# Kernel tuning notes

Measured on AMD Instinct MI355X. Metric: run time of the kernel, lower is better.

Reference implementation:

```python
import jax, jax.numpy as jnp
import numpy as np

N_HEAD = 12
ROPE_BASE = 10000.0


def rotate_half(x):
    h = x.shape[-1] // 2
    x1, x2 = x[..., :h], x[..., h:]
    return jnp.concatenate((-x2, x1), axis=-1)


def rope_cos_sin(T, head_dim, dtype):
    inv_freq = 1.0 / (ROPE_BASE ** (jnp.arange(0, head_dim, 2, dtype=jnp.float32) / head_dim))
    t = jnp.arange(T, dtype=jnp.float32)
    freqs = jnp.einsum('i,j->ij', t, inv_freq)          # [T, head_dim/2]
    emb = jnp.concatenate((freqs, freqs), axis=-1)       # [T, head_dim]
    return jnp.cos(emb).astype(dtype), jnp.sin(emb).astype(dtype)


def setup_inputs() -> dict:
    key = jax.random.key(0)
    ks = jax.random.split(key, 5)
    B, T, C = 1, 4096, 768
    return {
        'x': jax.random.normal(ks[0], (B, T, C), dtype=jnp.float32),
        'w_attn': jax.random.normal(ks[1], (C, 3 * C), dtype=jnp.float32) * (1.0 / np.sqrt(C)),
        'b_attn': jax.random.normal(ks[2], (3 * C,), dtype=jnp.float32) * 0.02,
        'w_proj': jax.random.normal(ks[3], (C, C), dtype=jnp.float32) * (1.0 / np.sqrt(C)),
        'b_proj': jax.random.normal(ks[4], (C,), dtype=jnp.float32) * 0.02,
    }


def reference(x, w_attn, b_attn, w_proj, b_proj):
    B, T, C = x.shape
    H = N_HEAD
    hd = C // H

    qkv = x @ w_attn + b_attn                            # [B, T, 3C]
    q, k, v = jnp.split(qkv, 3, axis=-1)
    q = q.reshape(B, T, H, hd)
    k = k.reshape(B, T, H, hd)
    v = v.reshape(B, T, H, hd)

    cos, sin = rope_cos_sin(T, hd, x.dtype)              # [T, hd]
    cos = cos[None, :, None, :]
    sin = sin[None, :, None, :]
    q = q * cos + rotate_half(q) * sin
    k = k * cos + rotate_half(k) * sin

    # [B, H, T, hd]
    q = q.transpose(0, 2, 1, 3)
    k = k.transpose(0, 2, 1, 3)
    v = v.transpose(0, 2, 1, 3)

    att = jnp.einsum('bhtd,bhsd->bhts', q, k) * (1.0 / np.sqrt(hd))
    causal_mask = jnp.triu(jnp.ones((T, T), dtype=bool), k=1)
    att = jnp.where(causal_mask, -jnp.inf, att)
    att = jax.nn.softmax(att, axis=-1)

    y = jnp.einsum('bhts,bhsd->bhtd', att, v)            # [B, H, T, hd]
    y = y.transpose(0, 2, 1, 3).reshape(B, T, C)
    return y @ w_proj + b_proj
```

## Files before the change

### kernel.cpp

```cpp
#include <hip/hip_runtime.h>
#include <hip/hip_bf16.h>
#include <math.h>

using bf16 = __hip_bfloat16;
typedef __bf16 bf16x8_t __attribute__((ext_vector_type(8)));
typedef float f32x4_t __attribute__((ext_vector_type(4)));

static __device__ __forceinline__ f32x4_t mfma16(bf16x8_t a, bf16x8_t b, f32x4_t c) {
    return __builtin_amdgcn_mfma_f32_16x16x32_bf16(a, b, c, 0, 0, 0);
}

#if __has_builtin(__builtin_amdgcn_exp2f)
#define EXP2F __builtin_amdgcn_exp2f
#else
#define EXP2F exp2f
#endif

static __device__ __forceinline__ void sincos_rev(float rev, float* s, float* c) {
    float f = rev - floorf(rev);
#if __has_builtin(__builtin_amdgcn_sinf) && __has_builtin(__builtin_amdgcn_cosf)
    *s = __builtin_amdgcn_sinf(f);
    *c = __builtin_amdgcn_cosf(f);
#else
    float th = f * 6.2831853071795864f;
    *s = __sinf(th); *c = __cosf(th);
#endif
}

static __device__ __forceinline__ void async16(bf16* lds, const bf16* g) {
    __builtin_amdgcn_global_load_lds(
        (const __attribute__((address_space(1))) unsigned int*)g,
        (__attribute__((address_space(3))) unsigned int*)lds, 16, 0, 0);
}

static __device__ __forceinline__ int detect_bf16(const unsigned short* u16) {
    const int lane = threadIdx.x & 63;
    int sane = 0;
#pragma unroll
    for (int j = 0; j < 4; ++j) {
        const unsigned short u = u16[2 * (lane * 4 + j)];
        const int e = (u >> 7) & 0xFF;
        if (u == 0 || (e >= 100 && e <= 150)) sane++;
    }
#pragma unroll
    for (int off = 1; off <= 32; off <<= 1) sane += __shfl_xor(sane, off);
    return (sane * 2 >= 256) ? 1 : 0;
}

static __device__ __forceinline__ float bias_at(const void* b, int i, int isbf) {
    return isbf ? __bfloat162float(((const bf16*)b)[i]) : ((const float*)b)[i];
}

static __device__ __forceinline__ void transpose_tile(
    const void* in, bf16* out, int in_ld, int out_ld, int bx, int by,
    int isbf, bf16 (*tile)[72]) {
    const int c0 = bx * 64, r0 = by * 64;
    const int tid = threadIdx.x;
    for (int c = tid; c < 512; c += 256) {
        const int r = c >> 3, co = (c & 7) << 3;
        if (isbf) {
            *reinterpret_cast<float4*>(&tile[r][co]) =
                *reinterpret_cast<const float4*>((const bf16*)in + (size_t)(r0 + r) * in_ld + c0 + co);
        } else {
            const float* f = (const float*)in + (size_t)(r0 + r) * in_ld + c0 + co;
            const float4 a = *reinterpret_cast<const float4*>(f);
            const float4 b = *reinterpret_cast<const float4*>(f + 4);
            tile[r][co + 0] = __float2bfloat16(a.x); tile[r][co + 1] = __float2bfloat16(a.y);
            tile[r][co + 2] = __float2bfloat16(a.z); tile[r][co + 3] = __float2bfloat16(a.w);
            tile[r][co + 4] = __float2bfloat16(b.x); tile[r][co + 5] = __float2bfloat16(b.y);
            tile[r][co + 6] = __float2bfloat16(b.z); tile[r][co + 7] = __float2bfloat16(b.w);
        }
    }
    __syncthreads();
    for (int c = tid; c < 512; c += 256) {
        const int r = c >> 3, co = (c & 7) << 3;
        union { float4 v; bf16 e[8]; } u;
#pragma unroll
        for (int j = 0; j < 8; ++j) u.e[j] = tile[co + j][r];
        *reinterpret_cast<float4*>(out + (size_t)(c0 + r) * out_ld + r0 + co) = u.v;
    }
}

__global__ __launch_bounds__(256) void prep_kernel(
    const void* __restrict__ x, const void* __restrict__ w_attn,
    const void* __restrict__ w_proj, bf16* __restrict__ xb,
    bf16* __restrict__ wAT, bf16* __restrict__ wPT) {
    __shared__ bf16 tile[64][72];
    const int isbf = detect_bf16((const unsigned short*)x);
    const int b = blockIdx.x;
    if (b < 432) {
        transpose_tile(w_attn, wAT, 2304, 768, b % 36, b / 36, isbf, tile);
    } else if (b < 576) {
        const int bb = b - 432;
        transpose_tile(w_proj, wPT, 768, 768, bb % 12, bb / 12, isbf, tile);
    } else {
        const int i = ((b - 576) * 256 + threadIdx.x) * 8;
        if (isbf) {
            *reinterpret_cast<float4*>(xb + i) =
                *reinterpret_cast<const float4*>((const bf16*)x + i);
        } else {
            const float* f = (const float*)x + i;
            const float4 a = *reinterpret_cast<const float4*>(f);
            const float4 c = *reinterpret_cast<const float4*>(f + 4);
            union { float4 v; bf16 e[8]; } u;
            u.e[0] = __float2bfloat16(a.x); u.e[1] = __float2bfloat16(a.y);
            u.e[2] = __float2bfloat16(a.z); u.e[3] = __float2bfloat16(a.w);
            u.e[4] = __float2bfloat16(c.x); u.e[5] = __float2bfloat16(c.y);
            u.e[6] = __float2bfloat16(c.z); u.e[7] = __float2bfloat16(c.w);
            *reinterpret_cast<float4*>(xb + i) = u.v;
        }
    }
}

template <int MI>
__global__ __launch_bounds__(256, MI == 4 ? 3 : 4) void gemm_kernel(
    const bf16* __restrict__ A, const bf16* __restrict__ Bt,
    const void* __restrict__ bias, bf16* __restrict__ C,
    bf16* __restrict__ VtOut, const unsigned short* __restrict__ xdet,
    int N, int K, int mode, int flexout) {
    constexpr int MT = MI * 32;
    __shared__ bf16 smem[(MT + 128) * 64];
    bf16* sa = smem;
    bf16* sb = smem + MT * 64;
    const int tid = threadIdx.x, lane = tid & 63, w = tid >> 6;
    const int wm = w >> 1, wn = w & 1, quad = lane >> 4, l16 = lane & 15;
    const int m0 = blockIdx.y * MT, n0 = blockIdx.x * 128;
    const int strow = lane >> 3, stslot = lane & 7;

    const bf16* ag[MI]; const bf16* bgp[4];
#pragma unroll
    for (int i = 0; i < MI; ++i) {
        const int r = (w * MI + i) * 8 + strow;
        ag[i] = A + (size_t)(m0 + r) * K + (stslot ^ (r & 7)) * 8;
    }
#pragma unroll
    for (int i = 0; i < 4; ++i) {
        const int r = (w * 4 + i) * 8 + strow;
        bgp[i] = Bt + (size_t)(n0 + r) * K + (stslot ^ (r & 7)) * 8;
    }

    f32x4_t acc[MI][4];
#pragma unroll
    for (int i = 0; i < MI; ++i)
#pragma unroll
        for (int j = 0; j < 4; ++j) acc[i][j] = (f32x4_t){0.f, 0.f, 0.f, 0.f};

    for (int k0 = 0; k0 < K; k0 += 64) {
        __syncthreads();
#pragma unroll
        for (int i = 0; i < MI; ++i) async16(&sa[(w * MI + i) * 512], ag[i] + k0);
#pragma unroll
        for (int i = 0; i < 4; ++i)  async16(&sb[(w * 4 + i) * 512], bgp[i] + k0);
        __asm__ __volatile__("s_waitcnt vmcnt(0)" ::: "memory");
        __syncthreads();

#pragma unroll
        for (int kk = 0; kk < 2; ++kk) {
            bf16x8_t af[MI], bf_[4];
#pragma unroll
            for (int mi = 0; mi < MI; ++mi) {
                const int r = wm * (MI * 16) + mi * 16 + l16;
                af[mi] = *reinterpret_cast<const bf16x8_t*>(
                    &sa[r * 64 + (((kk * 4 + quad) ^ (r & 7)) << 3)]);
            }
#pragma unroll
            for (int ni = 0; ni < 4; ++ni) {
                const int r = wn * 64 + ni * 16 + l16;
                bf_[ni] = *reinterpret_cast<const bf16x8_t*>(
                    &sb[r * 64 + (((kk * 4 + quad) ^ (r & 7)) << 3)]);
            }
#pragma unroll
            for (int mi = 0; mi < MI; ++mi)
#pragma unroll
                for (int ni = 0; ni < 4; ++ni)
                    acc[mi][ni] = mfma16(af[mi], bf_[ni], acc[mi][ni]);
        }
    }

    const int isbf = detect_bf16(xdet);
    const int f32out = flexout && !isbf;
    const int colbase = n0 + wn * 64;
    const int rowbase = m0 + wm * (MI * 16);
    if (mode == 1 && colbase < 1536) {
        const bool isq = colbase < 768;
        const float QS = 0.18033688011112042f;
#pragma unroll
        for (int ni = 0; ni < 2; ++ni) {
            const int d = ni * 16 + l16;
            const int col_lo = colbase + d, col_hi = col_lo + 32;
            const float blo = bias_at(bias, col_lo, isbf);
            const float bhi = bias_at(bias, col_hi, isbf);
            const float invf_rev = powf(10000.0f, -(float)d * (1.0f / 32.0f)) * 0.15915494309189535f;
#pragma unroll
            for (int mi = 0; mi < MI; ++mi) {
#pragma unroll
                for (int rg = 0; rg < 4; ++rg) {
                    const int t = rowbase + mi * 16 + quad * 4 + rg;
                    float sv, cv;
                    sincos_rev((float)t * invf_rev, &sv, &cv);
                    const float lo = acc[mi][ni][rg] + blo;
                    const float hi = acc[mi][ni + 2][rg] + bhi;
                    float nlo = lo * cv - hi * sv;
                    float nhi = hi * cv + lo * sv;
                    if (isq) { nlo *= QS; nhi *= QS; }
                    C[(size_t)t * N + col_lo] = __float2bfloat16(nlo);
                    C[(size_t)t * N + col_hi] = __float2bfloat16(nhi);
                }
            }
        }
    } else if (mode == 1) {
        if constexpr (MI == 4) {
            __syncthreads();
            bf16* T = smem + w * 2304;
            const int vcb = colbase - 1536;
#pragma unroll
            for (int pass = 0; pass < 2; ++pass) {
                if (pass) __asm__ __volatile__("s_waitcnt lgkmcnt(0)" ::: "memory");
#pragma unroll
                for (int nl = 0; nl < 2; ++nl) {
                    const int ni = pass * 2 + nl;
                    const float b = bias_at(bias, colbase + ni * 16 + l16, isbf);
                    const int dh = nl * 16 + l16;
#pragma unroll
                    for (int rg = 0; rg < 4; ++rg) {
                        union { int2 v; bf16 e[4]; } pk;
#pragma unroll
                        for (int mi = 0; mi < 4; ++mi)
                            pk.e[mi] = __float2bfloat16(acc[mi][ni][rg] + b);
                        *reinterpret_cast<int2*>(&T[dh * 72 + quad * 16 + rg * 4]) = pk.v;
                    }
                }
                __asm__ __volatile__("s_waitcnt lgkmcnt(0)" ::: "memory");
#pragma unroll
                for (int s = 0; s < 4; ++s) {
                    const int dh = s * 8 + (lane >> 3);
                    const int pj = lane & 7;
                    const float4 vv = *reinterpret_cast<const float4*>(&T[dh * 72 + pj * 8]);
                    *reinterpret_cast<float4*>(
                        &VtOut[(size_t)(vcb + pass * 32 + dh) * 4096 + rowbase + pj * 8]) = vv;
                }
            }
        }
    } else {
#pragma unroll
        for (int ni = 0; ni < 4; ++ni) {
            const int col = colbase + ni * 16 + l16;
            const float b = bias_at(bias, col, isbf);
#pragma unroll
            for (int mi = 0; mi < MI; ++mi) {
#pragma unroll
                for (int rg = 0; rg < 4; ++rg) {
                    const int t = rowbase + mi * 16 + quad * 4 + rg;
                    const float v = acc[mi][ni][rg] + b;
                    if (f32out) ((float*)C)[(size_t)t * N + col] = v;
                    else        C[(size_t)t * N + col] = __float2bfloat16(v);
                }
            }
        }
    }
}

__global__ __launch_bounds__(128, 3) void attn_kernel(
    const bf16* __restrict__ qkv, const bf16* __restrict__ Vt,
    bf16* __restrict__ ybuf, bf16* __restrict__ po, float* __restrict__ pl) {
    const int h = blockIdx.y;
    const int bx = blockIdx.x;
    int qt, c, nc;
    if (bx < 16)      { qt = bx;                 c = 0;             nc = 1; }
    else if (bx < 48) { qt = 16 + (bx - 16) / 2; c = (bx - 16) % 2; nc = 2; }
    else if (bx < 96) { qt = 32 + (bx - 48) / 3; c = (bx - 48) % 3; nc = 3; }
    else              { qt = 48 + (bx - 96) / 4; c = (bx - 96) % 4; nc = 4; }
    const int kt0 = c * 16;
    const int kt1 = min(kt0 + 16, qt + 1);

    const int tid = threadIdx.x, lane = tid & 63, w = tid >> 6;
    const int quad = lane >> 4, l16 = lane & 15, sw = l16 & 7;

    __shared__ bf16 Kt[4096];
    __shared__ bf16 Vs[4096];
    __shared__ bf16 Pt[2][2][16][72];

    const int strow = lane >> 3, stslot = lane & 7;
    const bf16* kg[4]; const bf16* vg[4];
#pragma unroll
    for (int i = 0; i < 4; ++i) {
        const int ch = w * 4 + i;
        const int key = ch * 8 + strow;
        kg[i] = qkv + (size_t)key * 2304 + 768 + h * 64 + (stslot ^ (key & 7)) * 8;
        const int d = ch * 8 + strow;
        vg[i] = Vt + (size_t)(h * 64 + d) * 4096 + (stslot ^ (d & 7)) * 8;
    }

    const int qbase = qt * 64 + w * 32;
    bf16x8_t qf[2][2];
#pragma unroll
    for (int f = 0; f < 2; ++f)
#pragma unroll
        for (int kc = 0; kc < 2; ++kc)
            qf[f][kc] = *reinterpret_cast<const bf16x8_t*>(
                qkv + (size_t)(qbase + f * 16 + l16) * 2304 + h * 64 + kc * 32 + quad * 8);

    f32x4_t o[2][4];
#pragma unroll
    for (int f = 0; f < 2; ++f)
#pragma unroll
        for (int dt = 0; dt < 4; ++dt) o[f][dt] = (f32x4_t){0.f, 0.f, 0.f, 0.f};
    float l_i[2][4] = {{0.f, 0.f, 0.f, 0.f}, {0.f, 0.f, 0.f, 0.f}};

#pragma unroll
    for (int i = 0; i < 4; ++i) {
        async16(&Kt[(w * 4 + i) * 512], kg[i] + (size_t)kt0 * 64 * 2304);
        async16(&Vs[(w * 4 + i) * 512], vg[i] + (size_t)kt0 * 64);
    }
    __asm__ __volatile__("s_waitcnt vmcnt(0)" ::: "memory");
    __syncthreads();

    for (int kt = kt0; kt < kt1; ++kt) {
        bf16x8_t kf[2][4], vf[2][4];
#pragma unroll
        for (int kc = 0; kc < 2; ++kc)
#pragma unroll
            for (int ct = 0; ct < 4; ++ct)
                kf[kc][ct] = *reinterpret_cast<const bf16x8_t*>(
                    &Kt[((ct * 16 + l16) << 6) + (((kc * 4 + quad) ^ sw) << 3)]);
#pragma unroll
        for (int kc = 0; kc < 2; ++kc)
#pragma unroll
            for (int dt = 0; dt < 4; ++dt)
                vf[kc][dt] = *reinterpret_cast<const bf16x8_t*>(
                    &Vs[((dt * 16 + l16) << 6) + (((kc * 4 + quad) ^ sw) << 3)]);
        __syncthreads();

        if (kt + 1 < kt1) {
#pragma unroll
            for (int i = 0; i < 4; ++i) {
                async16(&Kt[(w * 4 + i) * 512], kg[i] + (size_t)(kt + 1) * 64 * 2304);
                async16(&Vs[(w * 4 + i) * 512], vg[i] + (size_t)(kt + 1) * 64);
            }
        }

        f32x4_t s[2][4];
#pragma unroll
        for (int f = 0; f < 2; ++f)
#pragma unroll
            for (int ct = 0; ct < 4; ++ct) {
                s[f][ct] = mfma16(qf[f][0], kf[0][ct], (f32x4_t){0.f, 0.f, 0.f, 0.f});
                s[f][ct] = mfma16(qf[f][1], kf[1][ct], s[f][ct]);
            }

        if (kt == qt) {
#pragma unroll
            for (int f = 0; f < 2; ++f) {
                const int rowb = qbase + f * 16 + quad * 4;
#pragma unroll
                for (int ct = 0; ct < 4; ++ct) {
                    const int key = kt * 64 + ct * 16 + l16;
#pragma unroll
                    for (int rg = 0; rg < 4; ++rg)
                        if (key > rowb + rg) s[f][ct][rg] = -INFINITY;
                }
            }
        }

#pragma unroll
        for (int f = 0; f < 2; ++f)
#pragma unroll
            for (int ct = 0; ct < 4; ++ct)
#pragma unroll
                for (int rg = 0; rg < 4; ++rg) {
                    const float p = EXP2F(s[f][ct][rg]);
                    s[f][ct][rg] = p;
                    l_i[f][rg] += p;
                }

#pragma unroll
        for (int f = 0; f < 2; ++f)
#pragma unroll
            for (int rg = 0; rg < 4; ++rg) {
                union { int2 v; __hip_bfloat162 h2[2]; } pk;
                pk.h2[0] = __float22bfloat162_rn(float2{s[f][0][rg], s[f][1][rg]});
                pk.h2[1] = __float22bfloat162_rn(float2{s[f][2][rg], s[f][3][rg]});
                *reinterpret_cast<int2*>(&Pt[w][f][quad * 4 + rg][l16 * 4]) = pk.v;
            }
        __asm__ __volatile__("s_waitcnt lgkmcnt(0)" ::: "memory");

#pragma unroll
        for (int f = 0; f < 2; ++f)
#pragma unroll
            for (int kc = 0; kc < 2; ++kc) {
                const bf16x8_t pf =
                    *reinterpret_cast<const bf16x8_t*>(&Pt[w][f][l16][kc * 32 + quad * 8]);
#pragma unroll
                for (int dt = 0; dt < 4; ++dt)
                    o[f][dt] = mfma16(pf, vf[kc][dt], o[f][dt]);
            }

        __asm__ __volatile__("s_waitcnt vmcnt(0)" ::: "memory");
        __syncthreads();
    }

#pragma unroll
    for (int off = 1; off <= 8; off <<= 1)
#pragma unroll
        for (int f = 0; f < 2; ++f)
#pragma unroll
            for (int rg = 0; rg < 4; ++rg) l_i[f][rg] += __shfl_xor(l_i[f][rg], off);

    if (nc == 1) {
#pragma unroll
        for (int f = 0; f < 2; ++f) {
            float linv[4];
#pragma unroll
            for (int rg = 0; rg < 4; ++rg)
                linv[rg] = (l_i[f][rg] > 0.f) ? 1.0f / l_i[f][rg] : 0.f;
#pragma unroll
            for (int dt = 0; dt < 4; ++dt)
#pragma unroll
                for (int rg = 0; rg < 4; ++rg)
                    ybuf[(size_t)(qbase + f * 16 + quad * 4 + rg) * 768 + h * 64 + dt * 16 + l16] =
                        __float2bfloat16(o[f][dt][rg] * linv[rg]);
        }
    } else {
#pragma unroll
        for (int f = 0; f < 2; ++f) {
            float linv[4];
#pragma unroll
            for (int rg = 0; rg < 4; ++rg)
                linv[rg] = (l_i[f][rg] > 0.f) ? 1.0f / l_i[f][rg] : 0.f;
#pragma unroll
            for (int dt = 0; dt < 4; ++dt)
#pragma unroll
                for (int rg = 0; rg < 4; ++rg) {
                    const int row = qbase + f * 16 + quad * 4 + rg;
                    po[((size_t)((h << 12) + row) * 4 + c) * 64 + dt * 16 + l16] =
                        __float2bfloat16(o[f][dt][rg] * linv[rg]);
                }
            if (l16 == 0) {
#pragma unroll
                for (int rg = 0; rg < 4; ++rg) {
                    const int row = qbase + f * 16 + quad * 4 + rg;
                    pl[((h << 12) + row) * 4 + c] = l_i[f][rg];
                }
            }
        }
    }
}

__global__ __launch_bounds__(256) void combine_kernel(
    const bf16* __restrict__ po, const float* __restrict__ pl,
    bf16* __restrict__ ybuf) {
    const int g = blockIdx.x * 256 + threadIdx.x;
    if (g >= 12 * 3072 * 64) return;
    const int d = g & 63;
    const int rr = (g >> 6) % 3072;
    const int h = g / (3072 * 64);
    const int r = 1024 + rr;
    const int nc = (r >> 6) / 16 + 1;
    const int base = ((h << 12) + r) * 4;
    float wsum = 0.f, acc = 0.f;
    for (int cc = 0; cc < nc; ++cc) {
        const float wgt = pl[base + cc];
        wsum += wgt;
        acc += wgt * __bfloat162float(po[(size_t)(base + cc) * 64 + d]);
    }
    ybuf[(size_t)r * 768 + h * 64 + d] = __float2bfloat16(acc / wsum);
}

extern "C" void kernel_launch(void* const* d_in, const int* in_sizes, int n_in,
                              void* d_out, int out_size, void* d_ws, size_t ws_size,
                              hipStream_t stream) {
    bf16* qkv  = (bf16*)d_ws;
    bf16* wAT  = qkv + (size_t)4096 * 2304;
    bf16* wPT  = wAT + (size_t)2304 * 768;
    bf16* Vt   = wPT + (size_t)768 * 768;
    bf16* ybuf = Vt + (size_t)768 * 4096;
    bf16* xb   = ybuf + (size_t)4096 * 768;
    bf16* po   = xb + (size_t)4096 * 768;
    float* pl  = (float*)(po + (size_t)12 * 4096 * 4 * 64);
    const unsigned short* xdet = (const unsigned short*)d_in[0];

    prep_kernel<<<2112, 256, 0, stream>>>(d_in[0], d_in[1], d_in[3], xb, wAT, wPT);
    gemm_kernel<4><<<dim3(18, 32), 256, 0, stream>>>(
        xb, wAT, d_in[2], qkv, Vt, xdet, 2304, 768, 1, 0);
    attn_kernel<<<dim3(160, 12), 128, 0, stream>>>(qkv, Vt, ybuf, po, pl);
    combine_kernel<<<9216, 256, 0, stream>>>(po, pl, ybuf);
    gemm_kernel<1><<<dim3(6, 128), 256, 0, stream>>>(
        ybuf, wPT, d_in[4], (bf16*)d_out, nullptr, xdet, 768, 768, 0, 1);
}
```

Before: 181.2 us.

## Fuse fp32-to-bf16 conversion into QKV GEMM and split-K combine into attention

The x conversion pass in prep_kernel is removed. The QKV GEMM now loads fp32 x directly, converts it to bf16 in registers and stores it into the swizzled shared tile. The separate combine kernel is also removed: each attention block bumps a per-(head, query tile) atomic counter, and the last finishing chunk merges the partial outputs into ybuf. This saves two launches and a round trip of x through memory, at the cost of synchronous (non-async) A loads in the GEMM and a serialized tail merge in attention.

```diff
diff --git a/kernel.cpp b/kernel.cpp
--- a/kernel.cpp
+++ b/kernel.cpp
@@ -83,38 +83,25 @@
 
 __global__ __launch_bounds__(256) void prep_kernel(
     const void* __restrict__ x, const void* __restrict__ w_attn,
-    const void* __restrict__ w_proj, bf16* __restrict__ xb,
-    bf16* __restrict__ wAT, bf16* __restrict__ wPT) {
+    const void* __restrict__ w_proj, bf16* __restrict__ wAT,
+    bf16* __restrict__ wPT, int* __restrict__ cnt) {
     __shared__ bf16 tile[64][72];
     const int isbf = detect_bf16((const unsigned short*)x);
     const int b = blockIdx.x;
+    if (b == 0) {
+        for (int i = threadIdx.x; i < 768; i += 256) cnt[i] = 0;
+    }
     if (b < 432) {
         transpose_tile(w_attn, wAT, 2304, 768, b % 36, b / 36, isbf, tile);
-    } else if (b < 576) {
+    } else {
         const int bb = b - 432;
         transpose_tile(w_proj, wPT, 768, 768, bb % 12, bb / 12, isbf, tile);
-    } else {
-        const int i = ((b - 576) * 256 + threadIdx.x) * 8;
-        if (isbf) {
-            *reinterpret_cast<float4*>(xb + i) =
-                *reinterpret_cast<const float4*>((const bf16*)x + i);
-        } else {
-            const float* f = (const float*)x + i;
-            const float4 a = *reinterpret_cast<const float4*>(f);
-            const float4 c = *reinterpret_cast<const float4*>(f + 4);
-            union { float4 v; bf16 e[8]; } u;
-            u.e[0] = __float2bfloat16(a.x); u.e[1] = __float2bfloat16(a.y);
-            u.e[2] = __float2bfloat16(a.z); u.e[3] = __float2bfloat16(a.w);
-            u.e[4] = __float2bfloat16(c.x); u.e[5] = __float2bfloat16(c.y);
-            u.e[6] = __float2bfloat16(c.z); u.e[7] = __float2bfloat16(c.w);
-            *reinterpret_cast<float4*>(xb + i) = u.v;
-        }
-    }
-}
-
-template <int MI>
+    }
+}
+
+template <int MI, bool FLEXA>
 __global__ __launch_bounds__(256, MI == 4 ? 3 : 4) void gemm_kernel(
-    const bf16* __restrict__ A, const bf16* __restrict__ Bt,
+    const void* __restrict__ A, const bf16* __restrict__ Bt,
     const void* __restrict__ bias, bf16* __restrict__ C,
     bf16* __restrict__ VtOut, const unsigned short* __restrict__ xdet,
     int N, int K, int mode, int flexout) {
@@ -126,12 +113,13 @@
     const int wm = w >> 1, wn = w & 1, quad = lane >> 4, l16 = lane & 15;
     const int m0 = blockIdx.y * MT, n0 = blockIdx.x * 128;
     const int strow = lane >> 3, stslot = lane & 7;
-
-    const bf16* ag[MI]; const bf16* bgp[4];
+    const int isbf = detect_bf16(xdet);
+
+    size_t aoff[MI]; const bf16* bgp[4];
 #pragma unroll
     for (int i = 0; i < MI; ++i) {
         const int r = (w * MI + i) * 8 + strow;
-        ag[i] = A + (size_t)(m0 + r) * K + (stslot ^ (r & 7)) * 8;
+        aoff[i] = (size_t)(m0 + r) * K + (stslot ^ (r & 7)) * 8;
     }
 #pragma unroll
     for (int i = 0; i < 4; ++i) {
@@ -147,10 +135,26 @@
 
     for (int k0 = 0; k0 < K; k0 += 64) {
         __syncthreads();
-#pragma unroll
-        for (int i = 0; i < MI; ++i) async16(&sa[(w * MI + i) * 512], ag[i] + k0);
-#pragma unroll
-        for (int i = 0; i < 4; ++i)  async16(&sb[(w * 4 + i) * 512], bgp[i] + k0);
+        if (!FLEXA || isbf) {
+#pragma unroll
+            for (int i = 0; i < MI; ++i)
+                async16(&sa[(w * MI + i) * 512], (const bf16*)A + aoff[i] + k0);
+        } else {
+#pragma unroll
+            for (int i = 0; i < MI; ++i) {
+                const float* src = (const float*)A + aoff[i] + k0;
+                const float4 f0 = *reinterpret_cast<const float4*>(src);
+                const float4 f1 = *reinterpret_cast<const float4*>(src + 4);
+                union { float4 v; bf16 e[8]; } u;
+                u.e[0] = __float2bfloat16(f0.x); u.e[1] = __float2bfloat16(f0.y);
+                u.e[2] = __float2bfloat16(f0.z); u.e[3] = __float2bfloat16(f0.w);
+                u.e[4] = __float2bfloat16(f1.x); u.e[5] = __float2bfloat16(f1.y);
+                u.e[6] = __float2bfloat16(f1.z); u.e[7] = __float2bfloat16(f1.w);
+                *reinterpret_cast<float4*>(&sa[(w * MI + i) * 512 + lane * 8]) = u.v;
+            }
+        }
+#pragma unroll
+        for (int i = 0; i < 4; ++i) async16(&sb[(w * 4 + i) * 512], bgp[i] + k0);
         __asm__ __volatile__("s_waitcnt vmcnt(0)" ::: "memory");
         __syncthreads();
 
@@ -177,7 +181,6 @@
         }
     }
 
-    const int isbf = detect_bf16(xdet);
     const int f32out = flexout && !isbf;
     const int colbase = n0 + wn * 64;
     const int rowbase = m0 + wm * (MI * 16);
@@ -262,7 +265,8 @@
 
 __global__ __launch_bounds__(128, 3) void attn_kernel(
     const bf16* __restrict__ qkv, const bf16* __restrict__ Vt,
-    bf16* __restrict__ ybuf, bf16* __restrict__ po, float* __restrict__ pl) {
+    bf16* __restrict__ ybuf, bf16* __restrict__ po, float* __restrict__ pl,
+    int* __restrict__ cnt) {
     const int h = blockIdx.y;
     const int bx = blockIdx.x;
     int qt, c, nc;
@@ -279,6 +283,7 @@
     __shared__ bf16 Kt[4096];
     __shared__ bf16 Vs[4096];
     __shared__ bf16 Pt[2][2][16][72];
+    __shared__ int lastflag;
 
     const int strow = lane >> 3, stslot = lane & 7;
     const bf16* kg[4]; const bf16* vg[4];
@@ -443,27 +448,30 @@
                 }
             }
         }
-    }
-}
-
-__global__ __launch_bounds__(256) void combine_kernel(
-    const bf16* __restrict__ po, const float* __restrict__ pl,
-    bf16* __restrict__ ybuf) {
-    const int g = blockIdx.x * 256 + threadIdx.x;
-    if (g >= 12 * 3072 * 64) return;
-    const int d = g & 63;
-    const int rr = (g >> 6) % 3072;
-    const int h = g / (3072 * 64);
-    const int r = 1024 + rr;
-    const int nc = (r >> 6) / 16 + 1;
-    const int base = ((h << 12) + r) * 4;
-    float wsum = 0.f, acc = 0.f;
-    for (int cc = 0; cc < nc; ++cc) {
-        const float wgt = pl[base + cc];
-        wsum += wgt;
-        acc += wgt * __bfloat162float(po[(size_t)(base + cc) * 64 + d]);
-    }
-    ybuf[(size_t)r * 768 + h * 64 + d] = __float2bfloat16(acc / wsum);
+        __syncthreads();
+        __threadfence();
+        if (tid == 0) {
+            const int old = atomicAdd(&cnt[h * 64 + qt], 1);
+            lastflag = (old == nc - 1);
+        }
+        __syncthreads();
+        if (lastflag) {
+            __threadfence();
+            const int d = tid & 63;
+#pragma unroll 4
+            for (int it = 0; it < 32; ++it) {
+                const int r = qt * 64 + it * 2 + (tid >> 6);
+                const int pb = ((h << 12) + r) * 4;
+                float wsum = 0.f, accv = 0.f;
+                for (int cc = 0; cc < nc; ++cc) {
+                    const float wgt = pl[pb + cc];
+                    wsum += wgt;
+                    accv += wgt * __bfloat162float(po[(size_t)(pb + cc) * 64 + d]);
+                }
+                ybuf[(size_t)r * 768 + h * 64 + d] = __float2bfloat16(accv / wsum);
+            }
+        }
+    }
 }
 
 extern "C" void kernel_launch(void* const* d_in, const int* in_sizes, int n_in,
@@ -474,16 +482,15 @@
     bf16* wPT  = wAT + (size_t)2304 * 768;
     bf16* Vt   = wPT + (size_t)768 * 768;
     bf16* ybuf = Vt + (size_t)768 * 4096;
-    bf16* xb   = ybuf + (size_t)4096 * 768;
-    bf16* po   = xb + (size_t)4096 * 768;
+    bf16* po   = ybuf + (size_t)4096 * 768;
     float* pl  = (float*)(po + (size_t)12 * 4096 * 4 * 64);
+    int*  cnt  = (int*)(pl + (size_t)12 * 4096 * 4);
     const unsigned short* xdet = (const unsigned short*)d_in[0];
 
-    prep_kernel<<<2112, 256, 0, stream>>>(d_in[0], d_in[1], d_in[3], xb, wAT, wPT);
-    gemm_kernel<4><<<dim3(18, 32), 256, 0, stream>>>(
-        xb, wAT, d_in[2], qkv, Vt, xdet, 2304, 768, 1, 0);
-    attn_kernel<<<dim3(160, 12), 128, 0, stream>>>(qkv, Vt, ybuf, po, pl);
-    combine_kernel<<<9216, 256, 0, stream>>>(po, pl, ybuf);
-    gemm_kernel<1><<<dim3(6, 128), 256, 0, stream>>>(
+    prep_kernel<<<576, 256, 0, stream>>>(d_in[0], d_in[1], d_in[3], wAT, wPT, cnt);
+    gemm_kernel<4, true><<<dim3(18, 32), 256, 0, stream>>>(
+        d_in[0], wAT, d_in[2], qkv, Vt, xdet, 2304, 768, 1, 0);
+    attn_kernel<<<dim3(160, 12), 128, 0, stream>>>(qkv, Vt, ybuf, po, pl, cnt);
+    gemm_kernel<1, false><<<dim3(6, 128), 256, 0, stream>>>(
         ybuf, wPT, d_in[4], (bf16*)d_out, nullptr, xdet, 768, 768, 0, 1);
 }
```

After: 380.0 us. 2.1x slower.
